# Kernel optimization log

Measured on AMD Instinct MI355X. Metric: run time of the kernel, lower is better.

The kernel has to match this reference:

```python
import jax, jax.numpy as jnp
import numpy as np

HEADS = 16
DIM_HEAD = 64
MAX_REL_POS = 16  # temporal_length


def setup_inputs() -> dict:
    key = jax.random.key(0)
    ks = jax.random.split(key, 8)
    B, T, D = 2048, 16, 1024
    inner = HEADS * DIM_HEAD  # 1024
    w = 0.02  # weight init scale for numerical stability
    return {
        "x": jax.random.normal(ks[0], (B, T, D), jnp.float32),
        "Wq": jax.random.normal(ks[1], (inner, D), jnp.float32) * w,
        "Wk": jax.random.normal(ks[2], (inner, D), jnp.float32) * w,
        "Wv": jax.random.normal(ks[3], (inner, D), jnp.float32) * w,
        "Wo": jax.random.normal(ks[4], (D, inner), jnp.float32) * w,
        "bo": jnp.zeros((D,), jnp.float32),
        "rel_k_table": jax.random.normal(ks[5], (2 * MAX_REL_POS + 1, DIM_HEAD), jnp.float32) * w,
        "rel_v_table": jax.random.normal(ks[6], (2 * MAX_REL_POS + 1, DIM_HEAD), jnp.float32) * w,
    }


def reference(x, Wq, Wk, Wv, Wo, bo, rel_k_table, rel_v_table):
    B, T, D = x.shape
    h, dh = HEADS, DIM_HEAD
    scale = dh ** -0.5

    def split_heads(t):  # [B,T,h*dh] -> [B*h,T,dh]
        return t.reshape(B, T, h, dh).transpose(0, 2, 1, 3).reshape(B * h, T, dh)

    q = split_heads(x @ Wq.T)
    k = split_heads(x @ Wk.T)
    v = split_heads(x @ Wv.T)

    sim = jnp.einsum('bid,bjd->bij', q, k) * scale

    # relative-position bias: idx[i,j] = clip(j-i, -L, L) + L
    r = jnp.arange(T)
    idx = jnp.clip(r[None, :] - r[:, None], -MAX_REL_POS, MAX_REL_POS) + MAX_REL_POS
    k2 = rel_k_table[idx]  # [T,T,dh]
    sim = sim + jnp.einsum('btd,tsd->bts', q, k2) * scale

    attn = jax.nn.softmax(sim, axis=-1)
    out = jnp.einsum('bij,bjd->bid', attn, v)
    v2 = rel_v_table[idx]  # [T,T,dh]
    out = out + jnp.einsum('bts,tsd->btd', attn, v2)

    out = out.reshape(B, h, T, dh).transpose(0, 2, 1, 3).reshape(B, T, h * dh)
    return out @ Wo.T + bo
```

## Files before the change

### kernel.cpp

```cpp
#include <hip/hip_runtime.h>

#define HEADS 16
#define DIM_HEAD 64
#define T_SEQ 16
#define D_MODEL 1024
#define MAX_REL 16

typedef _Float16 half8 __attribute__((ext_vector_type(8)));
typedef float f32x4 __attribute__((ext_vector_type(4)));

__global__ __launch_bounds__(256)
void cvt_f32_f16(const float* __restrict__ in, _Float16* __restrict__ out, int n8) {
  int i = blockIdx.x * blockDim.x + threadIdx.x;
  if (i >= n8) return;
  float4 a = ((const float4*)in)[2 * i];
  float4 b = ((const float4*)in)[2 * i + 1];
  half8 h;
  h[0] = (_Float16)a.x; h[1] = (_Float16)a.y;
  h[2] = (_Float16)a.z; h[3] = (_Float16)a.w;
  h[4] = (_Float16)b.x; h[5] = (_Float16)b.y;
  h[6] = (_Float16)b.z; h[7] = (_Float16)b.w;
  ((half8*)out)[i] = h;
}

__device__ __forceinline__ void gload_lds16(const _Float16* g, _Float16* l) {
  __builtin_amdgcn_global_load_lds(
      (const __attribute__((address_space(1))) unsigned int*)(uintptr_t)g,
      (__attribute__((address_space(3))) unsigned int*)(uintptr_t)l, 16, 0, 0);
}

template <bool OUT_F16>
__global__ __launch_bounds__(512, 2)
void gemm256(const _Float16* __restrict__ A, const _Float16* __restrict__ B,
             const float* __restrict__ bias, void* __restrict__ Cv,
             int M, int N, int K) {
  __shared__ _Float16 lds[2][2][2][128][64];
  const int tid = threadIdx.x;
  const int wave = tid >> 6, lane = tid & 63;
  const int wm = wave >> 2, wn = wave & 3;

  const int GN = N >> 8;
  const int nwg = gridDim.x;
  const int q = nwg >> 3, r = nwg & 7;
  {
  }
  const int xcd = blockIdx.x & 7, pos = blockIdx.x >> 3;
  const int wgid = (xcd < r ? xcd * (q + 1) : r * (q + 1) + (xcd - r) * q) + pos;
  const int bm = wgid / GN, bn = wgid % GN;

  const int fr = lane & 15;
  const int q4 = lane >> 4;
  const int l3 = lane >> 3;
  const int sl = (lane & 7) ^ l3;

  const _Float16* Ag = A + (size_t)(bm * 256) * K;
  const _Float16* Bg = B + (size_t)(bn * 256) * K;

  f32x4 acc[8][4];
#pragma unroll
  for (int m = 0; m < 8; ++m)
#pragma unroll
    for (int n = 0; n < 4; ++n) acc[m][n] = (f32x4){0.f, 0.f, 0.f, 0.f};

  auto stage_half = [&](int buf, int ab, int half, const _Float16* G, int k0) {
#pragma unroll
    for (int i = 0; i < 2; ++i) {
      int g = wave * 2 + i;
      const _Float16* src =
          G + (size_t)(half * 128 + g * 8 + l3) * K + k0 + sl * 8;
      gload_lds16(src, &lds[buf][ab][half][g * 8][0]);
    }
  };

  auto ldA = [&](int buf, int mf, int ks) {
    unsigned off = (unsigned)((mf * 16 + fr) * 128 + (ks * 4 + q4) * 16) ^
                   (unsigned)((fr & 7) << 4);
    return *(const half8*)((const char*)&lds[buf][0][wm][0][0] + off);
  };
  auto ldB = [&](int buf, int nf, int ks) {
    int rowB = wn * 64 + nf * 16 + fr;
    unsigned off = (unsigned)((rowB & 127) * 128 + (ks * 4 + q4) * 16) ^
                   (unsigned)((fr & 7) << 4);
    return *(const half8*)((const char*)&lds[buf][1][rowB >> 7][0][0] + off);
  };

#pragma unroll
  for (int h = 0; h < 2; ++h) {
    stage_half(0, 0, h, Ag, 0);
    stage_half(0, 1, h, Bg, 0);
  }
  asm volatile("s_waitcnt vmcnt(0)" ::: "memory");
  __builtin_amdgcn_s_barrier();

  const int NT = K >> 6;
  for (int t = 0; t < NT; ++t) {
    const int cur = t & 1, nxt = cur ^ 1;
    const bool pf = (t + 1 < NT);
    const int k1 = (t + 1) << 6;
    half8 bF[4][2];
#pragma unroll
    for (int p = 0; p < 4; ++p) {
      half8 aF[2][2];
#pragma unroll
      for (int i = 0; i < 2; ++i)
#pragma unroll
        for (int ks = 0; ks < 2; ++ks) aF[i][ks] = ldA(cur, p * 2 + i, ks);
      if (p == 0) {
#pragma unroll
        for (int nf = 0; nf < 4; ++nf)
#pragma unroll
          for (int ks = 0; ks < 2; ++ks) bF[nf][ks] = ldB(cur, nf, ks);
      }
      if (pf) {
        if (p == 0) {
          stage_half(nxt, 0, 0, Ag, k1);
          stage_half(nxt, 0, 1, Ag, k1);
        } else if (p == 1) {
          stage_half(nxt, 1, 0, Bg, k1);
          stage_half(nxt, 1, 1, Bg, k1);
        }
      }
      __builtin_amdgcn_s_barrier();
      asm volatile("s_waitcnt lgkmcnt(0)" ::: "memory");
      __builtin_amdgcn_sched_barrier(0);
      __builtin_amdgcn_s_setprio(1);
#pragma unroll
      for (int i = 0; i < 2; ++i)
#pragma unroll
        for (int nf = 0; nf < 4; ++nf)
#pragma unroll
          for (int ks = 0; ks < 2; ++ks)
            acc[p * 2 + i][nf] = __builtin_amdgcn_mfma_f32_16x16x32_f16(
                aF[i][ks], bF[nf][ks], acc[p * 2 + i][nf], 0, 0, 0);
      __builtin_amdgcn_s_setprio(0);
      __builtin_amdgcn_sched_barrier(0);
      if (p == 3) asm volatile("s_waitcnt vmcnt(0)" ::: "memory");
      __builtin_amdgcn_s_barrier();
    }
  }

  const int row_l = q4 * 4;
#pragma unroll
  for (int mf = 0; mf < 8; ++mf) {
#pragma unroll
    for (int nf = 0; nf < 4; ++nf) {
      int col = bn * 256 + wn * 64 + nf * 16 + fr;
#pragma unroll
      for (int r4 = 0; r4 < 4; ++r4) {
        int row = bm * 256 + wm * 128 + mf * 16 + row_l + r4;
        if (OUT_F16) {
          ((_Float16*)Cv)[(size_t)row * N + col] = (_Float16)acc[mf][nf][r4];
        } else {
          ((float*)Cv)[(size_t)row * N + col] = acc[mf][nf][r4] + bias[col];
        }
      }
    }
  }
}

__global__ __launch_bounds__(256)
void attn_mfma(const _Float16* __restrict__ QKV,
               const float* __restrict__ relk, const float* __restrict__ relv,
               _Float16* __restrict__ O) {
  __shared__ _Float16 RK[32][72];
  __shared__ _Float16 RVt[64][40];
  __shared__ _Float16 PB[4][16][72];
  __shared__ _Float16 VtP[4][64][40];

  const int tid = threadIdx.x;
  const int wave = tid >> 6, lane = tid & 63;

  {
    int m = tid >> 3;
    int d0 = (tid & 7) * 8;
    float4 a = *(const float4*)(relk + m * 64 + d0);
    float4 b = *(const float4*)(relk + m * 64 + d0 + 4);
    half8 hk;
    hk[0] = (_Float16)a.x; hk[1] = (_Float16)a.y;
    hk[2] = (_Float16)a.z; hk[3] = (_Float16)a.w;
    hk[4] = (_Float16)b.x; hk[5] = (_Float16)b.y;
    hk[6] = (_Float16)b.z; hk[7] = (_Float16)b.w;
    *(half8*)&RK[m][d0] = hk;
    float4 c = *(const float4*)(relv + m * 64 + d0);
    float4 d = *(const float4*)(relv + m * 64 + d0 + 4);
    RVt[d0 + 0][m] = (_Float16)c.x; RVt[d0 + 1][m] = (_Float16)c.y;
    RVt[d0 + 2][m] = (_Float16)c.z; RVt[d0 + 3][m] = (_Float16)c.w;
    RVt[d0 + 4][m] = (_Float16)d.x; RVt[d0 + 5][m] = (_Float16)d.y;
    RVt[d0 + 6][m] = (_Float16)d.z; RVt[d0 + 7][m] = (_Float16)d.w;
  }

#pragma unroll
  for (int z = 0; z < 6; ++z) {
    int idx = z * 64 + lane;
    int row = idx / 24, cd = idx % 24;
    *(unsigned int*)&PB[wave][row][16 + 2 * cd] = 0u;
  }
#pragma unroll
  for (int z = 0; z < 8; ++z) {
    int idx = z * 64 + lane;
    int row = idx >> 3, cd = idx & 7;
    *(unsigned int*)&VtP[wave][row][16 + 2 * cd] = 0u;
  }

  const int bh = blockIdx.x * 4 + wave;
  const int b = bh >> 4, h = bh & 15;
  const size_t qbase = (size_t)(b * T_SEQ) * 3072 + h * 64;
  const int fr = lane & 15, fk8 = (lane >> 4) * 8;

  half8 aQ0 = *(const half8*)(QKV + qbase + (size_t)fr * 3072 + fk8);
  half8 aQ1 = *(const half8*)(QKV + qbase + (size_t)fr * 3072 + 32 + fk8);
  half8 bK0 = *(const half8*)(QKV + qbase + 1024 + (size_t)fr * 3072 + fk8);
  half8 bK1 = *(const half8*)(QKV + qbase + 1024 + (size_t)fr * 3072 + 32 + fk8);

  {
    const _Float16* vp = QKV + qbase + 2048 + (size_t)fr * 3072 + (lane >> 4) * 16;
    half8 v0 = *(const half8*)vp;
    half8 v1 = *(const half8*)(vp + 8);
    int d0 = (lane >> 4) * 16;
#pragma unroll
    for (int e = 0; e < 8; ++e) VtP[wave][d0 + e][fr] = v0[e];
#pragma unroll
    for (int e = 0; e < 8; ++e) VtP[wave][d0 + 8 + e][fr] = v1[e];
  }

  __syncthreads();

  f32x4 accS = {0.f, 0.f, 0.f, 0.f};
  accS = __builtin_amdgcn_mfma_f32_16x16x32_f16(aQ0, bK0, accS, 0, 0, 0);
  accS = __builtin_amdgcn_mfma_f32_16x16x32_f16(aQ1, bK1, accS, 0, 0, 0);

  half8 rk0a = *(const half8*)&RK[fr][fk8];
  half8 rk0b = *(const half8*)&RK[fr][32 + fk8];
  half8 rk1a = *(const half8*)&RK[16 + fr][fk8];
  half8 rk1b = *(const half8*)&RK[16 + fr][32 + fk8];
  f32x4 G0 = {0.f, 0.f, 0.f, 0.f}, G1 = {0.f, 0.f, 0.f, 0.f};
  G0 = __builtin_amdgcn_mfma_f32_16x16x32_f16(aQ0, rk0a, G0, 0, 0, 0);
  G0 = __builtin_amdgcn_mfma_f32_16x16x32_f16(aQ1, rk0b, G0, 0, 0, 0);
  G1 = __builtin_amdgcn_mfma_f32_16x16x32_f16(aQ0, rk1a, G1, 0, 0, 0);
  G1 = __builtin_amdgcn_mfma_f32_16x16x32_f16(aQ1, rk1b, G1, 0, 0, 0);

  const int ibase = (lane >> 4) * 4;
#pragma unroll
  for (int r = 0; r < 4; ++r) {
    const int i = ibase + r;
    const int ridx = fr - i + MAX_REL;
    const int src = (lane & 48) | (ridx & 15);
    float g0 = __shfl(G0[r], src);
    float g1 = __shfl(G1[r], src);
    float g = (ridx >= 16) ? g1 : g0;
    float s = (accS[r] + g) * 0.125f;
    float mx = s;
#pragma unroll
    for (int w = 8; w >= 1; w >>= 1) mx = fmaxf(mx, __shfl_xor(mx, w));
    float e = __expf(s - mx);
    float sum = e;
#pragma unroll
    for (int w = 8; w >= 1; w >>= 1) sum += __shfl_xor(sum, w);
    _Float16 ph = (_Float16)(e / sum);
    PB[wave][i][fr] = ph;
    PB[wave][i][32 + (fr - i + MAX_REL)] = ph;
  }

  half8 aP0 = *(const half8*)&PB[wave][fr][fk8];
  half8 aP1 = *(const half8*)&PB[wave][fr][32 + fk8];
  const size_t obase = (size_t)(b * T_SEQ) * D_MODEL + h * 64;
#pragma unroll
  for (int t = 0; t < 4; ++t) {
    half8 bv = *(const half8*)&VtP[wave][t * 16 + fr][fk8];
    half8 br = *(const half8*)&RVt[t * 16 + fr][fk8];
    f32x4 o = {0.f, 0.f, 0.f, 0.f};
    o = __builtin_amdgcn_mfma_f32_16x16x32_f16(aP0, bv, o, 0, 0, 0);
    o = __builtin_amdgcn_mfma_f32_16x16x32_f16(aP1, br, o, 0, 0, 0);
#pragma unroll
    for (int r = 0; r < 4; ++r)
      O[obase + (size_t)(ibase + r) * D_MODEL + t * 16 + fr] = (_Float16)o[r];
  }
}

extern "C" void kernel_launch(void* const* d_in, const int* in_sizes, int n_in,
                              void* d_out, int out_size, void* d_ws, size_t ws_size,
                              hipStream_t stream) {
  const float* x  = (const float*)d_in[0];
  const float* Wq = (const float*)d_in[1];
  const float* Wk = (const float*)d_in[2];
  const float* Wv = (const float*)d_in[3];
  const float* Wo = (const float*)d_in[4];
  const float* bo = (const float*)d_in[5];
  const float* rk = (const float*)d_in[6];
  const float* rv = (const float*)d_in[7];
  float* out = (float*)d_out;

  const int total_rows = 2048 * T_SEQ;
  const size_t wsz = (size_t)D_MODEL * D_MODEL;

  _Float16* Wqkvh = (_Float16*)d_ws;
  _Float16* Woh = Wqkvh + 3 * wsz;
  _Float16* chunk_base = Woh + wsz;

  {
    int n8 = (int)(wsz / 8);
    int blocks = (n8 + 255) / 256;
    cvt_f32_f16<<<blocks, 256, 0, stream>>>(Wq, Wqkvh, n8);
    cvt_f32_f16<<<blocks, 256, 0, stream>>>(Wk, Wqkvh + wsz, n8);
    cvt_f32_f16<<<blocks, 256, 0, stream>>>(Wv, Wqkvh + 2 * wsz, n8);
    cvt_f32_f16<<<blocks, 256, 0, stream>>>(Wo, Woh, n8);
  }

  const size_t per_row_bytes = (size_t)5120 * sizeof(_Float16);
  size_t avail = ws_size - (size_t)4 * wsz * sizeof(_Float16);
  size_t rows_fit = avail / per_row_bytes;
  int rows_c = (rows_fit > (size_t)total_rows) ? total_rows : (int)rows_fit;
  rows_c = (rows_c / 256) * 256;
  if (rows_c < 256) rows_c = 256;

  for (int r0 = 0; r0 < total_rows; r0 += rows_c) {
    int rc = total_rows - r0;
    if (rc > rows_c) rc = rows_c;

    _Float16* xh   = chunk_base;
    _Float16* QKVb = xh + (size_t)rows_c * 1024;
    _Float16* AO   = QKVb + (size_t)rows_c * 3072;

    {
      int n8 = rc * 128;
      cvt_f32_f16<<<(n8 + 255) / 256, 256, 0, stream>>>(
          x + (size_t)r0 * D_MODEL, xh, n8);
    }

    gemm256<true><<<(3072 / 256) * (rc / 256), 512, 0, stream>>>(
        xh, Wqkvh, nullptr, QKVb, rc, 3072, 1024);

    attn_mfma<<<rc / 4, 256, 0, stream>>>(QKVb, rk, rv, AO);

    gemm256<false><<<(1024 / 256) * (rc / 256), 512, 0, stream>>>(
        AO, Woh, bo, out + (size_t)r0 * D_MODEL, rc, 1024, 1024);
  }
}
```

Measured before the change: 414.6 us.

## Software-pipeline GEMM LDS fragment reads with ping-pong registers and one barrier per tile

Result: slower. 604.2 us (+45.7%).

```diff
diff --git a/kernel.cpp b/kernel.cpp
--- a/kernel.cpp
+++ b/kernel.cpp
@@ -42,8 +42,6 @@
   const int GN = N >> 8;
   const int nwg = gridDim.x;
   const int q = nwg >> 3, r = nwg & 7;
-  {
-  }
   const int xcd = blockIdx.x & 7, pos = blockIdx.x >> 3;
   const int wgid = (xcd < r ? xcd * (q + 1) : r * (q + 1) + (xcd - r) * q) + pos;
   const int bm = wgid / GN, bn = wgid % GN;
@@ -71,6 +69,12 @@
       gload_lds16(src, &lds[buf][ab][half][g * 8][0]);
     }
   };
+  auto stage_tile = [&](int buf, int k0) {
+    stage_half(buf, 0, 0, Ag, k0);
+    stage_half(buf, 0, 1, Ag, k0);
+    stage_half(buf, 1, 0, Bg, k0);
+    stage_half(buf, 1, 1, Bg, k0);
+  };
 
   auto ldA = [&](int buf, int mf, int ks) {
     unsigned off = (unsigned)((mf * 16 + fr) * 128 + (ks * 4 + q4) * 16) ^
@@ -84,59 +88,58 @@
     return *(const half8*)((const char*)&lds[buf][1][rowB >> 7][0][0] + off);
   };
 
-#pragma unroll
-  for (int h = 0; h < 2; ++h) {
-    stage_half(0, 0, h, Ag, 0);
-    stage_half(0, 1, h, Bg, 0);
-  }
-  asm volatile("s_waitcnt vmcnt(0)" ::: "memory");
-  __builtin_amdgcn_s_barrier();
+  half8 bFa[4][2], bFb[4][2], aA[2][2], aB[2][2];
+
+  auto rdA = [&](half8 (&dst)[2][2], int buf, int qd) {
+#pragma unroll
+    for (int i = 0; i < 2; ++i)
+#pragma unroll
+      for (int ks = 0; ks < 2; ++ks) dst[i][ks] = ldA(buf, qd * 2 + i, ks);
+  };
+  auto rdB = [&](half8 (&dst)[4][2], int buf) {
+#pragma unroll
+    for (int nf = 0; nf < 4; ++nf)
+#pragma unroll
+      for (int ks = 0; ks < 2; ++ks) dst[nf][ks] = ldB(buf, nf, ks);
+  };
+  auto mm = [&](int p, half8 (&af)[2][2], half8 (&bf)[4][2]) {
+    __builtin_amdgcn_s_setprio(1);
+#pragma unroll
+    for (int i = 0; i < 2; ++i)
+#pragma unroll
+      for (int nf = 0; nf < 4; ++nf)
+#pragma unroll
+        for (int ks = 0; ks < 2; ++ks)
+          acc[p * 2 + i][nf] = __builtin_amdgcn_mfma_f32_16x16x32_f16(
+              af[i][ks], bf[nf][ks], acc[p * 2 + i][nf], 0, 0, 0);
+    __builtin_amdgcn_s_setprio(0);
+  };
 
   const int NT = K >> 6;
-  for (int t = 0; t < NT; ++t) {
-    const int cur = t & 1, nxt = cur ^ 1;
-    const bool pf = (t + 1 < NT);
-    const int k1 = (t + 1) << 6;
-    half8 bF[4][2];
-#pragma unroll
-    for (int p = 0; p < 4; ++p) {
-      half8 aF[2][2];
-#pragma unroll
-      for (int i = 0; i < 2; ++i)
-#pragma unroll
-        for (int ks = 0; ks < 2; ++ks) aF[i][ks] = ldA(cur, p * 2 + i, ks);
-      if (p == 0) {
-#pragma unroll
-        for (int nf = 0; nf < 4; ++nf)
-#pragma unroll
-          for (int ks = 0; ks < 2; ++ks) bF[nf][ks] = ldB(cur, nf, ks);
-      }
-      if (pf) {
-        if (p == 0) {
-          stage_half(nxt, 0, 0, Ag, k1);
-          stage_half(nxt, 0, 1, Ag, k1);
-        } else if (p == 1) {
-          stage_half(nxt, 1, 0, Bg, k1);
-          stage_half(nxt, 1, 1, Bg, k1);
-        }
-      }
-      __builtin_amdgcn_s_barrier();
-      asm volatile("s_waitcnt lgkmcnt(0)" ::: "memory");
-      __builtin_amdgcn_sched_barrier(0);
-      __builtin_amdgcn_s_setprio(1);
-#pragma unroll
-      for (int i = 0; i < 2; ++i)
-#pragma unroll
-        for (int nf = 0; nf < 4; ++nf)
-#pragma unroll
-          for (int ks = 0; ks < 2; ++ks)
-            acc[p * 2 + i][nf] = __builtin_amdgcn_mfma_f32_16x16x32_f16(
-                aF[i][ks], bF[nf][ks], acc[p * 2 + i][nf], 0, 0, 0);
-      __builtin_amdgcn_s_setprio(0);
-      __builtin_amdgcn_sched_barrier(0);
-      if (p == 3) asm volatile("s_waitcnt vmcnt(0)" ::: "memory");
-      __builtin_amdgcn_s_barrier();
+
+  stage_tile(0, 0);
+  __syncthreads();
+  rdB(bFa, 0);
+  rdA(aA, 0, 0);
+
+  auto tile = [&](int t, int cur, half8 (&bf)[4][2], half8 (&bfn)[4][2]) {
+    const bool pf = (t + 1) < NT;
+    const int nxt = cur ^ 1;
+    if (pf) stage_tile(nxt, (t + 1) << 6);
+    rdA(aB, cur, 1); mm(0, aA, bf);
+    rdA(aA, cur, 2); mm(1, aB, bf);
+    rdA(aB, cur, 3); mm(2, aA, bf);
+    if (pf) {
+      __syncthreads();
+      rdB(bfn, nxt);
+      rdA(aA, nxt, 0);
     }
+    mm(3, aB, bf);
+  };
+
+  for (int t2 = 0; t2 < NT; t2 += 2) {
+    tile(t2, 0, bFa, bFb);
+    tile(t2 + 1, 1, bFb, bFa);
   }
 
   const int row_l = q4 * 4;
```

## Switch GEMM to 256x128 tiles with triple-buffered LDS prefetch two stages ahead

Applied to the files above, without the earlier changes.

Measured after the change: 448.7 us. +8.2%, slower.

```diff
diff --git a/kernel.cpp b/kernel.cpp
--- a/kernel.cpp
+++ b/kernel.cpp
@@ -31,19 +31,17 @@
 
 template <bool OUT_F16>
 __global__ __launch_bounds__(512, 2)
-void gemm256(const _Float16* __restrict__ A, const _Float16* __restrict__ B,
-             const float* __restrict__ bias, void* __restrict__ Cv,
-             int M, int N, int K) {
-  __shared__ _Float16 lds[2][2][2][128][64];
+void gemm3r(const _Float16* __restrict__ A, const _Float16* __restrict__ B,
+            const float* __restrict__ bias, void* __restrict__ Cv,
+            int M, int N, int K) {
+  __shared__ _Float16 lds[3][3][128][64];
   const int tid = threadIdx.x;
   const int wave = tid >> 6, lane = tid & 63;
   const int wm = wave >> 2, wn = wave & 3;
 
-  const int GN = N >> 8;
+  const int GN = N >> 7;
   const int nwg = gridDim.x;
   const int q = nwg >> 3, r = nwg & 7;
-  {
-  }
   const int xcd = blockIdx.x & 7, pos = blockIdx.x >> 3;
   const int wgid = (xcd < r ? xcd * (q + 1) : r * (q + 1) + (xcd - r) * q) + pos;
   const int bm = wgid / GN, bn = wgid % GN;
@@ -54,97 +52,122 @@
   const int sl = (lane & 7) ^ l3;
 
   const _Float16* Ag = A + (size_t)(bm * 256) * K;
-  const _Float16* Bg = B + (size_t)(bn * 256) * K;
-
-  f32x4 acc[8][4];
+  const _Float16* Bg = B + (size_t)(bn * 128) * K;
+
+  f32x4 acc[8][2];
 #pragma unroll
   for (int m = 0; m < 8; ++m)
 #pragma unroll
-    for (int n = 0; n < 4; ++n) acc[m][n] = (f32x4){0.f, 0.f, 0.f, 0.f};
-
-  auto stage_half = [&](int buf, int ab, int half, const _Float16* G, int k0) {
+    for (int n = 0; n < 2; ++n) acc[m][n] = (f32x4){0.f, 0.f, 0.f, 0.f};
+
+  auto stage_half = [&](int buf, int slab, const _Float16* G, int rowbase,
+                        int k0) {
 #pragma unroll
     for (int i = 0; i < 2; ++i) {
       int g = wave * 2 + i;
       const _Float16* src =
-          G + (size_t)(half * 128 + g * 8 + l3) * K + k0 + sl * 8;
-      gload_lds16(src, &lds[buf][ab][half][g * 8][0]);
-    }
+          G + (size_t)(rowbase + g * 8 + l3) * K + k0 + sl * 8;
+      gload_lds16(src, &lds[buf][slab][g * 8][0]);
+    }
+  };
+  auto stage_tile = [&](int buf, int k0) {
+    stage_half(buf, 0, Ag, 0, k0);
+    stage_half(buf, 1, Ag, 128, k0);
+    stage_half(buf, 2, Bg, 0, k0);
   };
 
   auto ldA = [&](int buf, int mf, int ks) {
     unsigned off = (unsigned)((mf * 16 + fr) * 128 + (ks * 4 + q4) * 16) ^
                    (unsigned)((fr & 7) << 4);
-    return *(const half8*)((const char*)&lds[buf][0][wm][0][0] + off);
+    return *(const half8*)((const char*)&lds[buf][wm][0][0] + off);
   };
   auto ldB = [&](int buf, int nf, int ks) {
-    int rowB = wn * 64 + nf * 16 + fr;
-    unsigned off = (unsigned)((rowB & 127) * 128 + (ks * 4 + q4) * 16) ^
+    int rowB = wn * 32 + nf * 16 + fr;
+    unsigned off = (unsigned)(rowB * 128 + (ks * 4 + q4) * 16) ^
                    (unsigned)((fr & 7) << 4);
-    return *(const half8*)((const char*)&lds[buf][1][rowB >> 7][0][0] + off);
+    return *(const half8*)((const char*)&lds[buf][2][0][0] + off);
   };
 
-#pragma unroll
-  for (int h = 0; h < 2; ++h) {
-    stage_half(0, 0, h, Ag, 0);
-    stage_half(0, 1, h, Bg, 0);
-  }
-  asm volatile("s_waitcnt vmcnt(0)" ::: "memory");
+  const int NT = K >> 6;
+
+  stage_tile(0, 0);
+  if (NT > 1) {
+    stage_tile(1, 64);
+    asm volatile("s_waitcnt vmcnt(6)" ::: "memory");
+  } else {
+    asm volatile("s_waitcnt vmcnt(0)" ::: "memory");
+  }
   __builtin_amdgcn_s_barrier();
 
-  const int NT = K >> 6;
+  int cur = 0, n2 = 2;
   for (int t = 0; t < NT; ++t) {
-    const int cur = t & 1, nxt = cur ^ 1;
-    const bool pf = (t + 1 < NT);
-    const int k1 = (t + 1) << 6;
-    half8 bF[4][2];
-#pragma unroll
-    for (int p = 0; p < 4; ++p) {
-      half8 aF[2][2];
-#pragma unroll
-      for (int i = 0; i < 2; ++i)
-#pragma unroll
-        for (int ks = 0; ks < 2; ++ks) aF[i][ks] = ldA(cur, p * 2 + i, ks);
-      if (p == 0) {
-#pragma unroll
-        for (int nf = 0; nf < 4; ++nf)
-#pragma unroll
-          for (int ks = 0; ks < 2; ++ks) bF[nf][ks] = ldB(cur, nf, ks);
-      }
-      if (pf) {
-        if (p == 0) {
-          stage_half(nxt, 0, 0, Ag, k1);
-          stage_half(nxt, 0, 1, Ag, k1);
-        } else if (p == 1) {
-          stage_half(nxt, 1, 0, Bg, k1);
-          stage_half(nxt, 1, 1, Bg, k1);
-        }
-      }
-      __builtin_amdgcn_s_barrier();
-      asm volatile("s_waitcnt lgkmcnt(0)" ::: "memory");
-      __builtin_amdgcn_sched_barrier(0);
-      __builtin_amdgcn_s_setprio(1);
-#pragma unroll
-      for (int i = 0; i < 2; ++i)
-#pragma unroll
-        for (int nf = 0; nf < 4; ++nf)
-#pragma unroll
-          for (int ks = 0; ks < 2; ++ks)
-            acc[p * 2 + i][nf] = __builtin_amdgcn_mfma_f32_16x16x32_f16(
-                aF[i][ks], bF[nf][ks], acc[p * 2 + i][nf], 0, 0, 0);
-      __builtin_amdgcn_s_setprio(0);
-      __builtin_amdgcn_sched_barrier(0);
-      if (p == 3) asm volatile("s_waitcnt vmcnt(0)" ::: "memory");
-      __builtin_amdgcn_s_barrier();
-    }
+    const bool pf2 = (t + 2) < NT;
+    const int k2 = (t + 2) << 6;
+    half8 aF[4][2], bF[2][2];
+
+#pragma unroll
+    for (int mf = 0; mf < 4; ++mf)
+#pragma unroll
+      for (int ks = 0; ks < 2; ++ks) aF[mf][ks] = ldA(cur, mf, ks);
+#pragma unroll
+    for (int nf = 0; nf < 2; ++nf)
+#pragma unroll
+      for (int ks = 0; ks < 2; ++ks) bF[nf][ks] = ldB(cur, nf, ks);
+    if (pf2) {
+      stage_half(n2, 0, Ag, 0, k2);
+      stage_half(n2, 1, Ag, 128, k2);
+    }
+    __builtin_amdgcn_s_barrier();
+    asm volatile("s_waitcnt lgkmcnt(0)" ::: "memory");
+    __builtin_amdgcn_sched_barrier(0);
+    __builtin_amdgcn_s_setprio(1);
+#pragma unroll
+    for (int mf = 0; mf < 4; ++mf)
+#pragma unroll
+      for (int nf = 0; nf < 2; ++nf)
+#pragma unroll
+        for (int ks = 0; ks < 2; ++ks)
+          acc[mf][nf] = __builtin_amdgcn_mfma_f32_16x16x32_f16(
+              aF[mf][ks], bF[nf][ks], acc[mf][nf], 0, 0, 0);
+    __builtin_amdgcn_s_setprio(0);
+    __builtin_amdgcn_sched_barrier(0);
+    __builtin_amdgcn_s_barrier();
+
+#pragma unroll
+    for (int mf = 0; mf < 4; ++mf)
+#pragma unroll
+      for (int ks = 0; ks < 2; ++ks) aF[mf][ks] = ldA(cur, mf + 4, ks);
+    if (pf2) stage_half(n2, 2, Bg, 0, k2);
+    __builtin_amdgcn_s_barrier();
+    asm volatile("s_waitcnt lgkmcnt(0)" ::: "memory");
+    __builtin_amdgcn_sched_barrier(0);
+    __builtin_amdgcn_s_setprio(1);
+#pragma unroll
+    for (int mf = 0; mf < 4; ++mf)
+#pragma unroll
+      for (int nf = 0; nf < 2; ++nf)
+#pragma unroll
+        for (int ks = 0; ks < 2; ++ks)
+          acc[mf + 4][nf] = __builtin_amdgcn_mfma_f32_16x16x32_f16(
+              aF[mf][ks], bF[nf][ks], acc[mf + 4][nf], 0, 0, 0);
+    __builtin_amdgcn_s_setprio(0);
+    __builtin_amdgcn_sched_barrier(0);
+    if (t + 1 < NT) {
+      if (pf2) asm volatile("s_waitcnt vmcnt(6)" ::: "memory");
+      else     asm volatile("s_waitcnt vmcnt(0)" ::: "memory");
+    }
+    __builtin_amdgcn_s_barrier();
+
+    cur = (cur == 2) ? 0 : cur + 1;
+    n2 = (n2 == 2) ? 0 : n2 + 1;
   }
 
   const int row_l = q4 * 4;
 #pragma unroll
   for (int mf = 0; mf < 8; ++mf) {
 #pragma unroll
-    for (int nf = 0; nf < 4; ++nf) {
-      int col = bn * 256 + wn * 64 + nf * 16 + fr;
+    for (int nf = 0; nf < 2; ++nf) {
+      int col = bn * 128 + wn * 32 + nf * 16 + fr;
 #pragma unroll
       for (int r4 = 0; r4 < 4; ++r4) {
         int row = bm * 256 + wm * 128 + mf * 16 + row_l + r4;
@@ -327,12 +350,12 @@
           x + (size_t)r0 * D_MODEL, xh, n8);
     }
 
-    gemm256<true><<<(3072 / 256) * (rc / 256), 512, 0, stream>>>(
+    gemm3r<true><<<(3072 / 128) * (rc / 256), 512, 0, stream>>>(
         xh, Wqkvh, nullptr, QKVb, rc, 3072, 1024);
 
     attn_mfma<<<rc / 4, 256, 0, stream>>>(QKVb, rk, rv, AO);
 
-    gemm256<false><<<(1024 / 256) * (rc / 256), 512, 0, stream>>>(
+    gemm3r<false><<<(1024 / 128) * (rc / 256), 512, 0, stream>>>(
         AO, Woh, bo, out + (size_t)r0 * D_MODEL, rc, 1024, 1024);
   }
 }
```

## Precompute fp16 relative tables once and relax GEMM and attention barriers

Applied to the files above, without the earlier changes.

New measurement: 420.0 us. Within noise of the previous version (+1.3%).

```diff
diff --git a/kernel.cpp b/kernel.cpp
--- a/kernel.cpp
+++ b/kernel.cpp
@@ -23,6 +23,30 @@
   ((half8*)out)[i] = h;
 }
 
+__global__ __launch_bounds__(256)
+void prep_tables(const float* __restrict__ relk, const float* __restrict__ relv,
+                 _Float16* __restrict__ RKh, _Float16* __restrict__ RVth) {
+  const int i = threadIdx.x;
+  {
+    int m = i >> 3, d0 = (i & 7) * 8;
+    float4 a = *(const float4*)(relk + m * 64 + d0);
+    float4 b = *(const float4*)(relk + m * 64 + d0 + 4);
+    half8 h;
+    h[0] = (_Float16)a.x; h[1] = (_Float16)a.y;
+    h[2] = (_Float16)a.z; h[3] = (_Float16)a.w;
+    h[4] = (_Float16)b.x; h[5] = (_Float16)b.y;
+    h[6] = (_Float16)b.z; h[7] = (_Float16)b.w;
+    *(half8*)(RKh + m * 64 + d0) = h;
+  }
+  {
+    int d = i >> 2, m0 = (i & 3) * 8;
+    half8 h;
+#pragma unroll
+    for (int e = 0; e < 8; ++e) h[e] = (_Float16)relv[(m0 + e) * 64 + d];
+    *(half8*)(RVth + d * 32 + m0) = h;
+  }
+}
+
 __device__ __forceinline__ void gload_lds16(const _Float16* g, _Float16* l) {
   __builtin_amdgcn_global_load_lds(
       (const __attribute__((address_space(1))) unsigned int*)(uintptr_t)g,
@@ -42,8 +66,6 @@
   const int GN = N >> 8;
   const int nwg = gridDim.x;
   const int q = nwg >> 3, r = nwg & 7;
-  {
-  }
   const int xcd = blockIdx.x & 7, pos = blockIdx.x >> 3;
   const int wgid = (xcd < r ? xcd * (q + 1) : r * (q + 1) + (xcd - r) * q) + pos;
   const int bm = wgid / GN, bn = wgid % GN;
@@ -112,15 +134,9 @@
           for (int ks = 0; ks < 2; ++ks) bF[nf][ks] = ldB(cur, nf, ks);
       }
       if (pf) {
-        if (p == 0) {
-          stage_half(nxt, 0, 0, Ag, k1);
-          stage_half(nxt, 0, 1, Ag, k1);
-        } else if (p == 1) {
-          stage_half(nxt, 1, 0, Bg, k1);
-          stage_half(nxt, 1, 1, Bg, k1);
-        }
+        if (p < 2) stage_half(nxt, 0, p, Ag, k1);
+        else       stage_half(nxt, 1, p - 2, Bg, k1);
       }
-      __builtin_amdgcn_s_barrier();
       asm volatile("s_waitcnt lgkmcnt(0)" ::: "memory");
       __builtin_amdgcn_sched_barrier(0);
       __builtin_amdgcn_s_setprio(1);
@@ -160,34 +176,13 @@
 
 __global__ __launch_bounds__(256)
 void attn_mfma(const _Float16* __restrict__ QKV,
-               const float* __restrict__ relk, const float* __restrict__ relv,
+               const _Float16* __restrict__ RKh, const _Float16* __restrict__ RVth,
                _Float16* __restrict__ O) {
-  __shared__ _Float16 RK[32][72];
-  __shared__ _Float16 RVt[64][40];
   __shared__ _Float16 PB[4][16][72];
   __shared__ _Float16 VtP[4][64][40];
 
   const int tid = threadIdx.x;
   const int wave = tid >> 6, lane = tid & 63;
-
-  {
-    int m = tid >> 3;
-    int d0 = (tid & 7) * 8;
-    float4 a = *(const float4*)(relk + m * 64 + d0);
-    float4 b = *(const float4*)(relk + m * 64 + d0 + 4);
-    half8 hk;
-    hk[0] = (_Float16)a.x; hk[1] = (_Float16)a.y;
-    hk[2] = (_Float16)a.z; hk[3] = (_Float16)a.w;
-    hk[4] = (_Float16)b.x; hk[5] = (_Float16)b.y;
-    hk[6] = (_Float16)b.z; hk[7] = (_Float16)b.w;
-    *(half8*)&RK[m][d0] = hk;
-    float4 c = *(const float4*)(relv + m * 64 + d0);
-    float4 d = *(const float4*)(relv + m * 64 + d0 + 4);
-    RVt[d0 + 0][m] = (_Float16)c.x; RVt[d0 + 1][m] = (_Float16)c.y;
-    RVt[d0 + 2][m] = (_Float16)c.z; RVt[d0 + 3][m] = (_Float16)c.w;
-    RVt[d0 + 4][m] = (_Float16)d.x; RVt[d0 + 5][m] = (_Float16)d.y;
-    RVt[d0 + 6][m] = (_Float16)d.z; RVt[d0 + 7][m] = (_Float16)d.w;
-  }
 
 #pragma unroll
   for (int z = 0; z < 6; ++z) {
@@ -211,6 +206,11 @@
   half8 aQ1 = *(const half8*)(QKV + qbase + (size_t)fr * 3072 + 32 + fk8);
   half8 bK0 = *(const half8*)(QKV + qbase + 1024 + (size_t)fr * 3072 + fk8);
   half8 bK1 = *(const half8*)(QKV + qbase + 1024 + (size_t)fr * 3072 + 32 + fk8);
+
+  half8 rk0a = *(const half8*)(RKh + fr * 64 + fk8);
+  half8 rk0b = *(const half8*)(RKh + fr * 64 + 32 + fk8);
+  half8 rk1a = *(const half8*)(RKh + (16 + fr) * 64 + fk8);
+  half8 rk1b = *(const half8*)(RKh + (16 + fr) * 64 + 32 + fk8);
 
   {
     const _Float16* vp = QKV + qbase + 2048 + (size_t)fr * 3072 + (lane >> 4) * 16;
@@ -223,16 +223,10 @@
     for (int e = 0; e < 8; ++e) VtP[wave][d0 + 8 + e][fr] = v1[e];
   }
 
-  __syncthreads();
-
   f32x4 accS = {0.f, 0.f, 0.f, 0.f};
   accS = __builtin_amdgcn_mfma_f32_16x16x32_f16(aQ0, bK0, accS, 0, 0, 0);
   accS = __builtin_amdgcn_mfma_f32_16x16x32_f16(aQ1, bK1, accS, 0, 0, 0);
 
-  half8 rk0a = *(const half8*)&RK[fr][fk8];
-  half8 rk0b = *(const half8*)&RK[fr][32 + fk8];
-  half8 rk1a = *(const half8*)&RK[16 + fr][fk8];
-  half8 rk1b = *(const half8*)&RK[16 + fr][32 + fk8];
   f32x4 G0 = {0.f, 0.f, 0.f, 0.f}, G1 = {0.f, 0.f, 0.f, 0.f};
   G0 = __builtin_amdgcn_mfma_f32_16x16x32_f16(aQ0, rk0a, G0, 0, 0, 0);
   G0 = __builtin_amdgcn_mfma_f32_16x16x32_f16(aQ1, rk0b, G0, 0, 0, 0);
@@ -267,7 +261,7 @@
 #pragma unroll
   for (int t = 0; t < 4; ++t) {
     half8 bv = *(const half8*)&VtP[wave][t * 16 + fr][fk8];
-    half8 br = *(const half8*)&RVt[t * 16 + fr][fk8];
+    half8 br = *(const half8*)(RVth + (t * 16 + fr) * 32 + fk8);
     f32x4 o = {0.f, 0.f, 0.f, 0.f};
     o = __builtin_amdgcn_mfma_f32_16x16x32_f16(aP0, bv, o, 0, 0, 0);
     o = __builtin_amdgcn_mfma_f32_16x16x32_f16(aP1, br, o, 0, 0, 0);
@@ -294,8 +288,10 @@
   const size_t wsz = (size_t)D_MODEL * D_MODEL;
 
   _Float16* Wqkvh = (_Float16*)d_ws;
-  _Float16* Woh = Wqkvh + 3 * wsz;
-  _Float16* chunk_base = Woh + wsz;
+  _Float16* Woh  = Wqkvh + 3 * wsz;
+  _Float16* RKh  = Woh + wsz;
+  _Float16* RVth = RKh + 2048;
+  _Float16* chunk_base = RVth + 2048;
 
   {
     int n8 = (int)(wsz / 8);
@@ -304,10 +300,11 @@
     cvt_f32_f16<<<blocks, 256, 0, stream>>>(Wk, Wqkvh + wsz, n8);
     cvt_f32_f16<<<blocks, 256, 0, stream>>>(Wv, Wqkvh + 2 * wsz, n8);
     cvt_f32_f16<<<blocks, 256, 0, stream>>>(Wo, Woh, n8);
+    prep_tables<<<1, 256, 0, stream>>>(rk, rv, RKh, RVth);
   }
 
   const size_t per_row_bytes = (size_t)5120 * sizeof(_Float16);
-  size_t avail = ws_size - (size_t)4 * wsz * sizeof(_Float16);
+  size_t avail = ws_size - (size_t)(4 * wsz + 4096) * sizeof(_Float16);
   size_t rows_fit = avail / per_row_bytes;
   int rows_c = (rows_fit > (size_t)total_rows) ? total_rows : (int)rows_fit;
   rows_c = (rows_c / 256) * 256;
@@ -330,7 +327,7 @@
     gemm256<true><<<(3072 / 256) * (rc / 256), 512, 0, stream>>>(
         xh, Wqkvh, nullptr, QKVb, rc, 3072, 1024);
 
-    attn_mfma<<<rc / 4, 256, 0, stream>>>(QKVb, rk, rv, AO);
+    attn_mfma<<<rc / 4, 256, 0, stream>>>(QKVb, RKh, RVth, AO);
 
     gemm256<false><<<(1024 / 256) * (rc / 256), 512, 0, stream>>>(
         AO, Woh, bo, out + (size_t)r0 * D_MODEL, rc, 1024, 1024);
```
